# Kernel optimization log

Measured on AMD Instinct MI355X. Metric: run time of the kernel, lower is better.

The kernel has to match this reference:

```python
import jax, jax.numpy as jnp
import numpy as np

EMBED = 1024
HEADS = 16
HEAD_DIM = EMBED // HEADS


def setup_inputs() -> dict:
    key = jax.random.key(0)
    ks = jax.random.split(key, 11)
    B, L, E = 2, 2048, EMBED
    s = 1.0 / np.sqrt(E)
    return {
        "query": jax.random.normal(ks[0], (B, L, E), jnp.float32),
        "key": jax.random.normal(ks[1], (B, L, E), jnp.float32),
        "value": jax.random.normal(ks[2], (B, L, E), jnp.float32),
        "Wq": jax.random.normal(ks[3], (E, E), jnp.float32) * s,
        "bq": jax.random.normal(ks[4], (E,), jnp.float32) * s,
        "Wk": jax.random.normal(ks[5], (E, E), jnp.float32) * s,
        "bk": jax.random.normal(ks[6], (E,), jnp.float32) * s,
        "Wv": jax.random.normal(ks[7], (E, E), jnp.float32) * s,
        "bv": jax.random.normal(ks[8], (E,), jnp.float32) * s,
        "Wo": jax.random.normal(ks[9], (E, E), jnp.float32) * s,
        "bo": jax.random.normal(ks[10], (E,), jnp.float32) * s,
    }


def reference(query, key, value, Wq, bq, Wk, bk, Wv, bv, Wo, bo):
    B, Lq, E = query.shape
    Lk = key.shape[1]
    # Linear projections (torch Linear: x @ W.T + b)
    q = (query @ Wq.T + bq).reshape(B, Lq, HEADS, HEAD_DIM).transpose(0, 2, 1, 3)
    k = (key @ Wk.T + bk).reshape(B, Lk, HEADS, HEAD_DIM).transpose(0, 2, 1, 3)
    v = (value @ Wv.T + bv).reshape(B, Lk, HEADS, HEAD_DIM).transpose(0, 2, 1, 3)
    # NOTE: original scales by sqrt(embed_size), not sqrt(head_dim)
    energy = jnp.einsum("bhqd,bhkd->bhqk", q, k) / jnp.sqrt(jnp.float32(E))
    attn = jax.nn.softmax(energy, axis=-1)
    out = jnp.einsum("bhqk,bhkd->bhqd", attn, v)  # [B,H,Lq,D]
    out = out.transpose(0, 2, 1, 3).reshape(B, Lq, E)
    return out @ Wo.T + bo
```

## Files before the change

### kernel.cpp

```cpp
#include <hip/hip_runtime.h>
#include <hip/hip_bf16.h>


typedef __attribute__((ext_vector_type(4))) float f32x4;
typedef __attribute__((ext_vector_type(16))) float f32x16;
typedef __attribute__((ext_vector_type(8))) short bf16x8;
typedef __attribute__((ext_vector_type(4))) short bf16x4;
typedef __attribute__((ext_vector_type(2))) unsigned int u32x2;

static __device__ __forceinline__ unsigned short f2bf(float f) {
  union { float f; unsigned int u; } a; a.f = f;
  unsigned int u = a.u;
  u += 0x7FFFu + ((u >> 16) & 1u);
  return (unsigned short)(u >> 16);
}

static __device__ __forceinline__ unsigned pack2(float lo, float hi) {
  unsigned a = __float_as_uint(lo) + 0x8000u;
  unsigned b = __float_as_uint(hi) + 0x8000u;
  return __builtin_amdgcn_perm(b, a, 0x07060302);
}

static __device__ __forceinline__ unsigned xchg32(unsigned x) {
  u32x2 r = __builtin_amdgcn_permlane32_swap(x, x, false, false);
  return x ^ r[0] ^ r[1];
}

#define AS1(p) ((const __attribute__((address_space(1))) void*)(p))
#define AS3(p) ((__attribute__((address_space(3))) void*)(p))

__global__ __launch_bounds__(256) void cvt_kernel(
    const float* __restrict__ q, const float* __restrict__ k, const float* __restrict__ v,
    const float* __restrict__ wq, const float* __restrict__ wk, const float* __restrict__ wv,
    const float* __restrict__ wo, short* __restrict__ ws) {
  long i = (long)blockIdx.x * 256 + threadIdx.x;
  long e = i * 8;
  const float* src; long off;
  if (e < 12582912) {
    int s = (int)(e >> 22);
    src = s == 0 ? q : (s == 1 ? k : v);
    off = e & 4194303;
  } else {
    long e2 = e - 12582912;
    int s = (int)(e2 >> 20);
    src = s == 0 ? wq : (s == 1 ? wk : (s == 2 ? wv : wo));
    off = e2 & 1048575;
  }
  f32x4 a = *(const f32x4*)(src + off);
  f32x4 b = *(const f32x4*)(src + off + 4);
  bf16x8 o;
  o[0] = (short)f2bf(a[0]); o[1] = (short)f2bf(a[1]);
  o[2] = (short)f2bf(a[2]); o[3] = (short)f2bf(a[3]);
  o[4] = (short)f2bf(b[0]); o[5] = (short)f2bf(b[1]);
  o[6] = (short)f2bf(b[2]); o[7] = (short)f2bf(b[3]);
  *(bf16x8*)(ws + e) = o;
}

__device__ __forceinline__ void gemm_tile(const short* __restrict__ A, const short* __restrict__ B,
                                          int m0, int n0, f32x4 acc[4][4],
                                          short* As, short* Bs) {
  const int t = threadIdx.x;
  const int lane = t & 63, w = t >> 6;
  const int wr = w >> 1, wc = w & 1;
  const int x = lane & 15, g = lane >> 4;
  const int lr = lane >> 3;
  const int lc = ((lane & 7) ^ lr) * 8;
  const int rswz = (x & 7) * 8;

#pragma unroll
  for (int fm = 0; fm < 4; fm++)
#pragma unroll
    for (int fn = 0; fn < 4; fn++)
#pragma unroll
      for (int r = 0; r < 4; r++) acc[fm][fn][r] = 0.0f;

  for (int k0 = 0; k0 < 1024; k0 += 64) {
    __syncthreads();
#pragma unroll
    for (int i = 0; i < 4; i++) {
      int ch = w * 4 + i;
      const short* ga = A + (long)(m0 + ch * 8 + lr) * 1024 + k0 + lc;
      __builtin_amdgcn_global_load_lds(AS1(ga), AS3(As + ch * 512), 16, 0, 0);
      const short* gb = B + (long)(n0 + ch * 8 + lr) * 1024 + k0 + lc;
      __builtin_amdgcn_global_load_lds(AS1(gb), AS3(Bs + ch * 512), 16, 0, 0);
    }
    __syncthreads();
#pragma unroll
    for (int ks = 0; ks < 2; ks++) {
      bf16x8 af[4], bfv[4];
#pragma unroll
      for (int f = 0; f < 4; f++) {
        int c = (ks * 32 + g * 8) ^ rswz;
        af[f]  = *(const bf16x8*)(As + (wr * 64 + f * 16 + x) * 64 + c);
        bfv[f] = *(const bf16x8*)(Bs + (wc * 64 + f * 16 + x) * 64 + c);
      }
#pragma unroll
      for (int fm = 0; fm < 4; fm++)
#pragma unroll
        for (int fn = 0; fn < 4; fn++)
          acc[fm][fn] = __builtin_amdgcn_mfma_f32_16x16x32_bf16(af[fm], bfv[fn], acc[fm][fn], 0, 0, 0);
    }
  }
}

__global__ __launch_bounds__(256) void proj_kernel(
    const short* __restrict__ Xq, const short* __restrict__ Xk, const short* __restrict__ Xv,
    const short* __restrict__ Wq, const short* __restrict__ Wk, const short* __restrict__ Wv,
    const float* __restrict__ bq, const float* __restrict__ bk, const float* __restrict__ bv,
    short* __restrict__ Qo, short* __restrict__ Ko, short* __restrict__ Vto) {
  __shared__ short As[8192], Bs[8192];
  const int z = blockIdx.z;
  const short* A = z == 0 ? Xq : (z == 1 ? Xk : Xv);
  const short* B = z == 0 ? Wq : (z == 1 ? Wk : Wv);
  const float* bias = z == 0 ? bq : (z == 1 ? bk : bv);
  const int m0 = blockIdx.y * 128, n0 = blockIdx.x * 128;
  f32x4 acc[4][4];
  gemm_tile(A, B, m0, n0, acc, As, Bs);

  const int lane = threadIdx.x & 63, w = threadIdx.x >> 6;
  const int wr = w >> 1, wc = w & 1, x = lane & 15, g = lane >> 4;

  if (z == 0) {
    const float scale = 0.04508422002778f;
#pragma unroll
    for (int fn = 0; fn < 4; fn++) {
      int n = n0 + wc * 64 + fn * 16 + x;
      float bb = bias[n];
      int h = n >> 6, d = n & 63;
#pragma unroll
      for (int fm = 0; fm < 4; fm++) {
        int mb = m0 + wr * 64 + fm * 16 + g * 4;
#pragma unroll
        for (int r = 0; r < 4; r++) {
          int m = mb + r;
          int b = m >> 11, l = m & 2047;
          float val = (acc[fm][fn][r] + bb) * scale;
          Qo[((long)((b * 16 + h) * 2048 + l)) * 64 + d] = (short)f2bf(val);
        }
      }
    }
  } else if (z == 1) {
#pragma unroll
    for (int fn = 0; fn < 4; fn++) {
      int n = n0 + wc * 64 + fn * 16 + x;
      float bb = bias[n];
      int h = n >> 6, d = n & 63;
#pragma unroll
      for (int fm = 0; fm < 4; fm++) {
        int mb = m0 + wr * 64 + fm * 16 + g * 4;
#pragma unroll
        for (int r = 0; r < 4; r++) {
          int m = mb + r;
          int b = m >> 11, kv = m & 2047;
          int ds = d ^ ((kv & 7) << 3);
          Ko[((long)((b * 16 + h) * 2048 + kv)) * 64 + ds] = (short)f2bf(acc[fm][fn][r] + bb);
        }
      }
    }
  } else {
#pragma unroll
    for (int fn = 0; fn < 4; fn++) {
      int n = n0 + wc * 64 + fn * 16 + x;
      float bb = bias[n];
      int h = n >> 6, d = n & 63;
#pragma unroll
      for (int fm = 0; fm < 4; fm++) {
        int mb = m0 + wr * 64 + fm * 16 + g * 4;
        int b = mb >> 11, kvb = mb & 2047;
        bf16x4 pk;
#pragma unroll
        for (int r = 0; r < 4; r++) pk[r] = (short)f2bf(acc[fm][fn][r] + bb);
        int kvs = (kvb & ~63) | ((kvb & 63) ^ ((d & 7) << 3));
        *(bf16x4*)(Vto + ((long)((b * 16 + h) * 64 + d)) * 2048 + kvs) = pk;
      }
    }
  }
}

__global__ __launch_bounds__(256, 2) void attn_kernel(
    const short* __restrict__ Qg, const short* __restrict__ Kg,
    const short* __restrict__ Vtg, short* __restrict__ Og) {
  __shared__ __align__(16) short Kl[2][8192];
  __shared__ __align__(16) short Vl[2][8192];
  const int t = threadIdx.x, w = t >> 6, lane = t & 63;
  const int col = lane & 31, hi = lane >> 5;
  const int bh = blockIdx.y;
  const int q0 = blockIdx.x * 128 + w * 32;
  const long hb = (long)bh * 2048 * 64;
  const int swz = (col & 7) * 8;

  bf16x8 qf[4];
#pragma unroll
  for (int ksl = 0; ksl < 4; ksl++)
    qf[ksl] = *(const bf16x8*)(Qg + hb + (long)(q0 + col) * 64 + ksl * 16 + hi * 8);

  f32x16 o0, o1;
#pragma unroll
  for (int i = 0; i < 16; i++) { o0[i] = 0.0f; o1[i] = 0.0f; }
  float l_r = 0.0f;

  auto stage = [&](int buf, int kv0) {
#pragma unroll
    for (int it = 0; it < 4; it++) {
      int cb = it * 256 + w * 64;
      const short* gk = Kg + hb + (long)kv0 * 64 + (cb + lane) * 8;
      __builtin_amdgcn_global_load_lds(AS1(gk), AS3(&Kl[buf][cb * 8]), 16, 0, 0);
      int c = cb + lane;
      const short* gv = Vtg + hb + (long)(c >> 4) * 2048 + kv0 + (c & 15) * 8;
      __builtin_amdgcn_global_load_lds(AS1(gv), AS3(&Vl[buf][cb * 8]), 16, 0, 0);
    }
  };

  stage(0, 0);
  __syncthreads();

  for (int ti = 0; ti < 16; ti++) {
    const int buf = ti & 1;
    if (ti < 15) stage(buf ^ 1, (ti + 1) * 128);

#pragma unroll
    for (int st = 0; st < 2; st++) {
      f32x16 s0, s1;
#pragma unroll
      for (int i = 0; i < 16; i++) { s0[i] = 0.0f; s1[i] = 0.0f; }
      __builtin_amdgcn_s_setprio(1);
#pragma unroll
      for (int ksl = 0; ksl < 4; ksl++) {
        int dcol = (ksl * 16 + hi * 8) ^ swz;
        bf16x8 a0 = *(const bf16x8*)(&Kl[buf][(st * 64 + col) * 64 + dcol]);
        bf16x8 a1 = *(const bf16x8*)(&Kl[buf][(st * 64 + col + 32) * 64 + dcol]);
        s0 = __builtin_amdgcn_mfma_f32_32x32x16_bf16(a0, qf[ksl], s0, 0, 0, 0);
        s1 = __builtin_amdgcn_mfma_f32_32x32x16_bf16(a1, qf[ksl], s1, 0, 0, 0);
      }
      __builtin_amdgcn_s_setprio(0);

#pragma unroll
      for (int i = 0; i < 16; i++) { s0[i] = __builtin_amdgcn_exp2f(s0[i]); }
#pragma unroll
      for (int i = 0; i < 16; i++) { s1[i] = __builtin_amdgcn_exp2f(s1[i]); }
      {
        float a0 = s0[0] + s0[1], a1 = s0[2] + s0[3], a2 = s0[4] + s0[5], a3 = s0[6] + s0[7];
        float a4 = s0[8] + s0[9], a5 = s0[10] + s0[11], a6 = s0[12] + s0[13], a7 = s0[14] + s0[15];
        float b0 = s1[0] + s1[1], b1 = s1[2] + s1[3], b2 = s1[4] + s1[5], b3 = s1[6] + s1[7];
        float b4 = s1[8] + s1[9], b5 = s1[10] + s1[11], b6 = s1[12] + s1[13], b7 = s1[14] + s1[15];
        float c0 = a0 + a1, c1 = a2 + a3, c2 = a4 + a5, c3 = a6 + a7;
        float c4 = b0 + b1, c5 = b2 + b3, c6 = b4 + b5, c7 = b6 + b7;
        float d0 = c0 + c1, d1 = c2 + c3, d2 = c4 + c5, d3 = c6 + c7;
        l_r += (d0 + d1) + (d2 + d3);
      }

#define PVSTEP(SEL, KS)                                                       \
      {                                                                       \
        unsigned pkA0 = pack2(SEL[8 * ((KS) & 1) + 0], SEL[8 * ((KS) & 1) + 1]); \
        unsigned pkA1 = pack2(SEL[8 * ((KS) & 1) + 2], SEL[8 * ((KS) & 1) + 3]); \
        unsigned pkB0 = pack2(SEL[8 * ((KS) & 1) + 4], SEL[8 * ((KS) & 1) + 5]); \
        unsigned pkB1 = pack2(SEL[8 * ((KS) & 1) + 6], SEL[8 * ((KS) & 1) + 7]); \
        unsigned own0 = hi ? pkB0 : pkA0, own1 = hi ? pkB1 : pkA1;            \
        unsigned oth0 = hi ? pkA0 : pkB0, oth1 = hi ? pkA1 : pkB1;            \
        unsigned r0 = xchg32(oth0);                                           \
        unsigned r1 = xchg32(oth1);                                           \
        union { unsigned u[4]; bf16x8 v; } pb;                                \
        pb.u[0] = hi ? r0 : own0; pb.u[1] = hi ? r1 : own1;                   \
        pb.u[2] = hi ? own0 : r0; pb.u[3] = hi ? own1 : r1;                   \
        const int vcol = ((KS) * 16 + hi * 8) ^ swz;                          \
        bf16x8 vb0 = *(const bf16x8*)(&Vl[buf][col * 128 + st * 64 + vcol]);  \
        bf16x8 vb1 = *(const bf16x8*)(&Vl[buf][(col + 32) * 128 + st * 64 + vcol]); \
        __builtin_amdgcn_s_setprio(1);                                        \
        o0 = __builtin_amdgcn_mfma_f32_32x32x16_bf16(vb0, pb.v, o0, 0, 0, 0); \
        o1 = __builtin_amdgcn_mfma_f32_32x32x16_bf16(vb1, pb.v, o1, 0, 0, 0); \
        __builtin_amdgcn_s_setprio(0);                                        \
      }
      PVSTEP(s0, 0)
      PVSTEP(s0, 1)
      PVSTEP(s1, 2)
      PVSTEP(s1, 3)
#undef PVSTEP
    }

    __syncthreads();
  }

  const float l_tot = l_r + __uint_as_float(xchg32(__float_as_uint(l_r)));
  const float inv = 1.0f / l_tot;
  const int b = bh >> 4, h = bh & 15;
  const long base = ((long)(b * 2048 + q0 + col) * 16 + h) * 64;
#pragma unroll
  for (int dh = 0; dh < 2; dh++) {
#pragma unroll
    for (int g2 = 0; g2 < 4; g2++) {
      float x0 = (dh ? o1[g2 * 4 + 0] : o0[g2 * 4 + 0]) * inv;
      float x1 = (dh ? o1[g2 * 4 + 1] : o0[g2 * 4 + 1]) * inv;
      float x2 = (dh ? o1[g2 * 4 + 2] : o0[g2 * 4 + 2]) * inv;
      float x3 = (dh ? o1[g2 * 4 + 3] : o0[g2 * 4 + 3]) * inv;
      u32x2 rr;
      rr[0] = (unsigned)f2bf(x0) | ((unsigned)f2bf(x1) << 16);
      rr[1] = (unsigned)f2bf(x2) | ((unsigned)f2bf(x3) << 16);
      int d = dh * 32 + g2 * 8 + hi * 4;
      *(u32x2*)(Og + base + d) = rr;
    }
  }
}

__global__ __launch_bounds__(256) void out_kernel(
    const short* __restrict__ O, const short* __restrict__ Wo,
    const float* __restrict__ bo, float* __restrict__ out) {
  __shared__ short As[8192], Bs[8192];
  const int m0 = blockIdx.y * 128, n0 = blockIdx.x * 128;
  f32x4 acc[4][4];
  gemm_tile(O, Wo, m0, n0, acc, As, Bs);
  const int lane = threadIdx.x & 63, w = threadIdx.x >> 6;
  const int wr = w >> 1, wc = w & 1, x = lane & 15, g = lane >> 4;
#pragma unroll
  for (int fn = 0; fn < 4; fn++) {
    int n = n0 + wc * 64 + fn * 16 + x;
    float bb = bo[n];
#pragma unroll
    for (int fm = 0; fm < 4; fm++) {
      int mb = m0 + wr * 64 + fm * 16 + g * 4;
#pragma unroll
      for (int r = 0; r < 4; r++)
        out[(long)(mb + r) * 1024 + n] = acc[fm][fn][r] + bb;
    }
  }
}

extern "C" void kernel_launch(void* const* d_in, const int* in_sizes, int n_in,
                              void* d_out, int out_size, void* d_ws, size_t ws_size,
                              hipStream_t stream) {
  const float* q  = (const float*)d_in[0];
  const float* k  = (const float*)d_in[1];
  const float* v  = (const float*)d_in[2];
  const float* wq = (const float*)d_in[3];
  const float* bq = (const float*)d_in[4];
  const float* wk = (const float*)d_in[5];
  const float* bk = (const float*)d_in[6];
  const float* wv = (const float*)d_in[7];
  const float* bv = (const float*)d_in[8];
  const float* wo = (const float*)d_in[9];
  const float* bo = (const float*)d_in[10];

  short* ws  = (short*)d_ws;
  short* Xq  = ws;
  short* Xk  = Xq + 4194304;
  short* Xv  = Xk + 4194304;
  short* Wqb = Xv + 4194304;
  short* Wkb = Wqb + 1048576;
  short* Wvb = Wkb + 1048576;
  short* Wob = Wvb + 1048576;
  short* Qb  = Wob + 1048576;
  short* Kb  = Qb + 4194304;
  short* Vtb = Kb + 4194304;
  short* Ob  = Vtb + 4194304;

  cvt_kernel<<<8192, 256, 0, stream>>>(q, k, v, wq, wk, wv, wo, ws);
  dim3 gp(8, 32, 3);
  proj_kernel<<<gp, 256, 0, stream>>>(Xq, Xk, Xv, Wqb, Wkb, Wvb, bq, bk, bv, Qb, Kb, Vtb);
  dim3 ga(16, 32);
  attn_kernel<<<ga, 256, 0, stream>>>(Qb, Kb, Vtb, Ob);
  dim3 gf(8, 32);
  out_kernel<<<gf, 256, 0, stream>>>(Ob, Wob, bo, (float*)d_out);
}
```

Before: 137.4 us.

## Load K/V tiles directly from global into registers, dropping LDS staging

The attention kernel stops staging K and V tiles through double-buffered shared memory with global_load_lds and barriers. Each wave now loads its K fragments straight from global memory into registers, software-pipelined one 64-key tile ahead, and loads V fragments inside the compute step. The XOR swizzle in the projection kernel's K/V output layout is removed to match. This removes LDS traffic and the block-wide __syncthreads, at the cost of each of the four waves re-reading the same K/V from global/L2 without sharing, and of V loads that are barely pipelined.

```diff
diff --git a/kernel.cpp b/kernel.cpp
--- a/kernel.cpp
+++ b/kernel.cpp
@@ -152,8 +152,7 @@
         for (int r = 0; r < 4; r++) {
           int m = mb + r;
           int b = m >> 11, kv = m & 2047;
-          int ds = d ^ ((kv & 7) << 3);
-          Ko[((long)((b * 16 + h) * 2048 + kv)) * 64 + ds] = (short)f2bf(acc[fm][fn][r] + bb);
+          Ko[((long)((b * 16 + h) * 2048 + kv)) * 64 + d] = (short)f2bf(acc[fm][fn][r] + bb);
         }
       }
     }
@@ -170,8 +169,7 @@
         bf16x4 pk;
 #pragma unroll
         for (int r = 0; r < 4; r++) pk[r] = (short)f2bf(acc[fm][fn][r] + bb);
-        int kvs = (kvb & ~63) | ((kvb & 63) ^ ((d & 7) << 3));
-        *(bf16x4*)(Vto + ((long)((b * 16 + h) * 64 + d)) * 2048 + kvs) = pk;
+        *(bf16x4*)(Vto + ((long)((b * 16 + h) * 64 + d)) * 2048 + kvb) = pk;
       }
     }
   }
@@ -180,14 +178,13 @@
 __global__ __launch_bounds__(256, 2) void attn_kernel(
     const short* __restrict__ Qg, const short* __restrict__ Kg,
     const short* __restrict__ Vtg, short* __restrict__ Og) {
-  __shared__ __align__(16) short Kl[2][8192];
-  __shared__ __align__(16) short Vl[2][8192];
   const int t = threadIdx.x, w = t >> 6, lane = t & 63;
   const int col = lane & 31, hi = lane >> 5;
   const int bh = blockIdx.y;
   const int q0 = blockIdx.x * 128 + w * 32;
   const long hb = (long)bh * 2048 * 64;
-  const int swz = (col & 7) * 8;
+  const short* Kb = Kg + hb;
+  const short* Vb = Vtg + hb;
 
   bf16x8 qf[4];
 #pragma unroll
@@ -199,85 +196,82 @@
   for (int i = 0; i < 16; i++) { o0[i] = 0.0f; o1[i] = 0.0f; }
   float l_r = 0.0f;
 
-  auto stage = [&](int buf, int kv0) {
-#pragma unroll
-    for (int it = 0; it < 4; it++) {
-      int cb = it * 256 + w * 64;
-      const short* gk = Kg + hb + (long)kv0 * 64 + (cb + lane) * 8;
-      __builtin_amdgcn_global_load_lds(AS1(gk), AS3(&Kl[buf][cb * 8]), 16, 0, 0);
-      int c = cb + lane;
-      const short* gv = Vtg + hb + (long)(c >> 4) * 2048 + kv0 + (c & 15) * 8;
-      __builtin_amdgcn_global_load_lds(AS1(gv), AS3(&Vl[buf][cb * 8]), 16, 0, 0);
+  auto loadK = [&](int n, bf16x8 (&kf)[8]) {
+    const long kvo = (long)(n & 31) * 64;
+#pragma unroll
+    for (int ksl = 0; ksl < 4; ksl++) {
+      kf[ksl]     = *(const bf16x8*)(Kb + (kvo + col) * 64 + ksl * 16 + hi * 8);
+      kf[4 + ksl] = *(const bf16x8*)(Kb + (kvo + col + 32) * 64 + ksl * 16 + hi * 8);
     }
   };
 
-  stage(0, 0);
-  __syncthreads();
-
-  for (int ti = 0; ti < 16; ti++) {
-    const int buf = ti & 1;
-    if (ti < 15) stage(buf ^ 1, (ti + 1) * 128);
-
-#pragma unroll
-    for (int st = 0; st < 2; st++) {
-      f32x16 s0, s1;
-#pragma unroll
-      for (int i = 0; i < 16; i++) { s0[i] = 0.0f; s1[i] = 0.0f; }
-      __builtin_amdgcn_s_setprio(1);
-#pragma unroll
-      for (int ksl = 0; ksl < 4; ksl++) {
-        int dcol = (ksl * 16 + hi * 8) ^ swz;
-        bf16x8 a0 = *(const bf16x8*)(&Kl[buf][(st * 64 + col) * 64 + dcol]);
-        bf16x8 a1 = *(const bf16x8*)(&Kl[buf][(st * 64 + col + 32) * 64 + dcol]);
-        s0 = __builtin_amdgcn_mfma_f32_32x32x16_bf16(a0, qf[ksl], s0, 0, 0, 0);
-        s1 = __builtin_amdgcn_mfma_f32_32x32x16_bf16(a1, qf[ksl], s1, 0, 0, 0);
-      }
-      __builtin_amdgcn_s_setprio(0);
-
-#pragma unroll
-      for (int i = 0; i < 16; i++) { s0[i] = __builtin_amdgcn_exp2f(s0[i]); }
-#pragma unroll
-      for (int i = 0; i < 16; i++) { s1[i] = __builtin_amdgcn_exp2f(s1[i]); }
-      {
-        float a0 = s0[0] + s0[1], a1 = s0[2] + s0[3], a2 = s0[4] + s0[5], a3 = s0[6] + s0[7];
-        float a4 = s0[8] + s0[9], a5 = s0[10] + s0[11], a6 = s0[12] + s0[13], a7 = s0[14] + s0[15];
-        float b0 = s1[0] + s1[1], b1 = s1[2] + s1[3], b2 = s1[4] + s1[5], b3 = s1[6] + s1[7];
-        float b4 = s1[8] + s1[9], b5 = s1[10] + s1[11], b6 = s1[12] + s1[13], b7 = s1[14] + s1[15];
-        float c0 = a0 + a1, c1 = a2 + a3, c2 = a4 + a5, c3 = a6 + a7;
-        float c4 = b0 + b1, c5 = b2 + b3, c6 = b4 + b5, c7 = b6 + b7;
-        float d0 = c0 + c1, d1 = c2 + c3, d2 = c4 + c5, d3 = c6 + c7;
-        l_r += (d0 + d1) + (d2 + d3);
-      }
+  auto compute = [&](int n, bf16x8 (&kf)[8]) {
+    const long kvo = (long)n * 64;
+    bf16x8 vf[8];
+#pragma unroll
+    for (int KS = 0; KS < 4; KS++) {
+      vf[KS]     = *(const bf16x8*)(Vb + (long)col * 2048 + kvo + KS * 16 + hi * 8);
+      vf[4 + KS] = *(const bf16x8*)(Vb + (long)(col + 32) * 2048 + kvo + KS * 16 + hi * 8);
+    }
+
+    f32x16 s0, s1;
+#pragma unroll
+    for (int i = 0; i < 16; i++) { s0[i] = 0.0f; s1[i] = 0.0f; }
+    __builtin_amdgcn_s_setprio(1);
+#pragma unroll
+    for (int ksl = 0; ksl < 4; ksl++) {
+      s0 = __builtin_amdgcn_mfma_f32_32x32x16_bf16(kf[ksl], qf[ksl], s0, 0, 0, 0);
+      s1 = __builtin_amdgcn_mfma_f32_32x32x16_bf16(kf[4 + ksl], qf[ksl], s1, 0, 0, 0);
+    }
+    __builtin_amdgcn_s_setprio(0);
+
+#pragma unroll
+    for (int i = 0; i < 16; i++) { s0[i] = __builtin_amdgcn_exp2f(s0[i]); }
+#pragma unroll
+    for (int i = 0; i < 16; i++) { s1[i] = __builtin_amdgcn_exp2f(s1[i]); }
+    {
+      float a0 = s0[0] + s0[1], a1 = s0[2] + s0[3], a2 = s0[4] + s0[5], a3 = s0[6] + s0[7];
+      float a4 = s0[8] + s0[9], a5 = s0[10] + s0[11], a6 = s0[12] + s0[13], a7 = s0[14] + s0[15];
+      float b0 = s1[0] + s1[1], b1 = s1[2] + s1[3], b2 = s1[4] + s1[5], b3 = s1[6] + s1[7];
+      float b4 = s1[8] + s1[9], b5 = s1[10] + s1[11], b6 = s1[12] + s1[13], b7 = s1[14] + s1[15];
+      float c0 = a0 + a1, c1 = a2 + a3, c2 = a4 + a5, c3 = a6 + a7;
+      float c4 = b0 + b1, c5 = b2 + b3, c6 = b4 + b5, c7 = b6 + b7;
+      float d0 = c0 + c1, d1 = c2 + c3, d2 = c4 + c5, d3 = c6 + c7;
+      l_r += (d0 + d1) + (d2 + d3);
+    }
 
 #define PVSTEP(SEL, KS)                                                       \
-      {                                                                       \
-        unsigned pkA0 = pack2(SEL[8 * ((KS) & 1) + 0], SEL[8 * ((KS) & 1) + 1]); \
-        unsigned pkA1 = pack2(SEL[8 * ((KS) & 1) + 2], SEL[8 * ((KS) & 1) + 3]); \
-        unsigned pkB0 = pack2(SEL[8 * ((KS) & 1) + 4], SEL[8 * ((KS) & 1) + 5]); \
-        unsigned pkB1 = pack2(SEL[8 * ((KS) & 1) + 6], SEL[8 * ((KS) & 1) + 7]); \
-        unsigned own0 = hi ? pkB0 : pkA0, own1 = hi ? pkB1 : pkA1;            \
-        unsigned oth0 = hi ? pkA0 : pkB0, oth1 = hi ? pkA1 : pkB1;            \
-        unsigned r0 = xchg32(oth0);                                           \
-        unsigned r1 = xchg32(oth1);                                           \
-        union { unsigned u[4]; bf16x8 v; } pb;                                \
-        pb.u[0] = hi ? r0 : own0; pb.u[1] = hi ? r1 : own1;                   \
-        pb.u[2] = hi ? own0 : r0; pb.u[3] = hi ? own1 : r1;                   \
-        const int vcol = ((KS) * 16 + hi * 8) ^ swz;                          \
-        bf16x8 vb0 = *(const bf16x8*)(&Vl[buf][col * 128 + st * 64 + vcol]);  \
-        bf16x8 vb1 = *(const bf16x8*)(&Vl[buf][(col + 32) * 128 + st * 64 + vcol]); \
-        __builtin_amdgcn_s_setprio(1);                                        \
-        o0 = __builtin_amdgcn_mfma_f32_32x32x16_bf16(vb0, pb.v, o0, 0, 0, 0); \
-        o1 = __builtin_amdgcn_mfma_f32_32x32x16_bf16(vb1, pb.v, o1, 0, 0, 0); \
-        __builtin_amdgcn_s_setprio(0);                                        \
-      }
-      PVSTEP(s0, 0)
-      PVSTEP(s0, 1)
-      PVSTEP(s1, 2)
-      PVSTEP(s1, 3)
+    {                                                                         \
+      unsigned pkA0 = pack2(SEL[8 * ((KS) & 1) + 0], SEL[8 * ((KS) & 1) + 1]); \
+      unsigned pkA1 = pack2(SEL[8 * ((KS) & 1) + 2], SEL[8 * ((KS) & 1) + 3]); \
+      unsigned pkB0 = pack2(SEL[8 * ((KS) & 1) + 4], SEL[8 * ((KS) & 1) + 5]); \
+      unsigned pkB1 = pack2(SEL[8 * ((KS) & 1) + 6], SEL[8 * ((KS) & 1) + 7]); \
+      unsigned own0 = hi ? pkB0 : pkA0, own1 = hi ? pkB1 : pkA1;              \
+      unsigned oth0 = hi ? pkA0 : pkB0, oth1 = hi ? pkA1 : pkB1;              \
+      unsigned r0 = xchg32(oth0);                                             \
+      unsigned r1 = xchg32(oth1);                                             \
+      union { unsigned u[4]; bf16x8 v; } pb;                                  \
+      pb.u[0] = hi ? r0 : own0; pb.u[1] = hi ? r1 : own1;                     \
+      pb.u[2] = hi ? own0 : r0; pb.u[3] = hi ? own1 : r1;                     \
+      __builtin_amdgcn_s_setprio(1);                                          \
+      o0 = __builtin_amdgcn_mfma_f32_32x32x16_bf16(vf[KS], pb.v, o0, 0, 0, 0);     \
+      o1 = __builtin_amdgcn_mfma_f32_32x32x16_bf16(vf[4 + KS], pb.v, o1, 0, 0, 0); \
+      __builtin_amdgcn_s_setprio(0);                                          \
+    }
+    PVSTEP(s0, 0)
+    PVSTEP(s0, 1)
+    PVSTEP(s1, 2)
+    PVSTEP(s1, 3)
 #undef PVSTEP
-    }
-
-    __syncthreads();
+  };
+
+  bf16x8 kA[8], kB[8];
+  loadK(0, kA);
+  for (int n = 0; n < 32; n += 2) {
+    loadK(n + 1, kB);
+    compute(n, kA);
+    loadK(n + 2, kA);
+    compute(n + 1, kB);
   }
 
   const float l_tot = l_r + __uint_as_float(xchg32(__float_as_uint(l_r)));
```

After: 206.0 us. 49.9% more time.
